# Kernel optimization log

Measured on AMD Instinct MI355X. Metric: run time of the kernel, lower is better.

## Reference

```python
import jax, jax.numpy as jnp
import numpy as np

N = 50000   # nodes
E = 800000  # edges (avg degree 16)
IN, H, OUT = 128, 128, 64


def setup_inputs() -> dict:
    key = jax.random.key(0)
    ks = jax.random.split(key, 8)

    def w(k, shape):
        fan_in = shape[0]
        return (jax.random.normal(k, shape, jnp.float32) / np.float32(np.sqrt(fan_in)))

    x = jax.random.normal(ks[0], (N, IN), jnp.float32)
    edge_index = jax.random.randint(ks[1], (2, E), 0, N, jnp.int64)
    return {
        "x": x,
        "edge_index": edge_index,
        "W1": w(ks[2], (IN, H)), "b1": jnp.zeros((H,), jnp.float32),
        "W2": w(ks[3], (H, H)),  "b2": jnp.zeros((H,), jnp.float32),
        "W3": w(ks[4], (H, H)),  "b3": jnp.zeros((H,), jnp.float32),
        "Wd1": w(ks[5], (H, H)), "bd1": jnp.zeros((H,), jnp.float32),
        "Wd2": w(ks[6], (H, OUT)), "bd2": jnp.zeros((OUT,), jnp.float32),
    }


def _gcn_conv(x, src, dst, norm, W, b):
    # x: [N, Cin] -> linear transform, gather along edges, normalized scatter-add
    h = x @ W                                   # [N, Cout]
    msg = h[src] * norm[:, None]                # [E+N, Cout]
    out = jax.ops.segment_sum(msg, dst, num_segments=N)
    return out + b


def reference(x, edge_index, W1, b1, W2, b2, W3, b3, Wd1, bd1, Wd2, bd2):
    # Add self-loops (PyG GCNConv default) and compute symmetric normalization.
    loops = jnp.arange(N, dtype=edge_index.dtype)
    src = jnp.concatenate([edge_index[0], loops])   # [E+N]
    dst = jnp.concatenate([edge_index[1], loops])   # [E+N]
    deg = jax.ops.segment_sum(jnp.ones_like(dst, dtype=x.dtype), dst, num_segments=N)
    dinv = jnp.where(deg > 0, jax.lax.rsqrt(deg), jnp.zeros_like(deg))
    norm = dinv[src] * dinv[dst]                    # [E+N]

    h = jax.nn.relu(_gcn_conv(x, src, dst, norm, W1, b1))
    h = jax.nn.relu(_gcn_conv(h, src, dst, norm, W2, b2))
    h = jax.nn.relu(_gcn_conv(h, src, dst, norm, W3, b3))

    h = jax.nn.relu(h @ Wd1 + bd1)
    return jax.nn.sigmoid(h @ Wd2 + bd2)            # [N, OUT]
```

## Files before the change

### kernel.cpp

```cpp
#include <hip/hip_runtime.h>
#include <hip/hip_bf16.h>
#include <hip/hip_fp16.h>

#define N_NODES 50000
#define N_EDGES 800000
#define C_H 128
#define C_OUT 64
#define NBLK 196
#define TSTRIDE 136
#define E_PAD 950272
#define MM_BLKS 782

typedef __attribute__((ext_vector_type(8))) short bf16x8;
typedef __attribute__((ext_vector_type(4))) float f32x4;

static __device__ __forceinline__ float bf_lo(unsigned int u) { return __uint_as_float(u << 16); }
static __device__ __forceinline__ float bf_hi(unsigned int u) { return __uint_as_float(u & 0xffff0000u); }
static __device__ __forceinline__ unsigned short f2bf(float f) {
    __hip_bfloat16 h = __float2bfloat16(f);
    return *(unsigned short*)&h;
}
static __device__ __forceinline__ unsigned int pack2(float a, float b) {
    return (unsigned int)f2bf(a) | ((unsigned int)f2bf(b) << 16);
}
static __device__ __forceinline__ unsigned short f2h_bits(float f) {
    union { __half h; unsigned short u; } c; c.h = __float2half_rn(f); return c.u;
}
static __device__ __forceinline__ float h_bits2f(unsigned short u) {
    union { __half h; unsigned short u; } c; c.u = u; return __half2float(c.h);
}

__global__ void prep_kernel(const int* __restrict__ dst, int* __restrict__ counts,
                            int* __restrict__ rank,
                            const float* __restrict__ W1, const float* __restrict__ W2,
                            const float* __restrict__ W3, const float* __restrict__ Wd1,
                            const float* __restrict__ Wd2,
                            unsigned short* __restrict__ P1, unsigned short* __restrict__ P2,
                            unsigned short* __restrict__ P3, unsigned short* __restrict__ Pd1,
                            unsigned short* __restrict__ Pd2,
                            unsigned int* __restrict__ epay) {
    int b = blockIdx.x;
    if (b < 3125) {
        int e = b * 256 + threadIdx.x;
        rank[e] = atomicAdd(&counts[dst[e]], 1);
    } else if (b < 3413) {
        int idx = (b - 3125) * 256 + threadIdx.x;
        if (idx < 4 * 16384) {
            int which = idx >> 14;
            int r = idx & 16383;
            const float* W = (which == 0) ? W1 : (which == 1) ? W2 : (which == 2) ? W3 : Wd1;
            unsigned short* P = (which == 0) ? P1 : (which == 1) ? P2 : (which == 2) ? P3 : Pd1;
            int j = r & 7, lane = (r >> 3) & 63, t = r >> 9;
            int nb = t & 7, kb = t >> 3;
            int k = kb * 32 + ((lane >> 4) << 3) + j;
            int n = nb * 16 + (lane & 15);
            P[r] = f2bf(W[(size_t)k * 128 + n]);
        } else {
            int r = idx - 65536;
            if (r < 8192) {
                int j = r & 7, lane = (r >> 3) & 63, t = r >> 9;
                int nb = t & 3, kb = t >> 2;
                int k = kb * 32 + ((lane >> 4) << 3) + j;
                int n = nb * 16 + (lane & 15);
                Pd2[r] = f2bf(Wd2[(size_t)k * 64 + n]);
            }
        }
    } else {
        int i = (b - 3413) * 256 + threadIdx.x;
        *(uint4*)(epay + (size_t)i * 4) = make_uint4(0, 0, 0, 0);
    }
}

__global__ void __launch_bounds__(256) scan1_kernel(const int* __restrict__ counts,
                                                    int* __restrict__ eblk,
                                                    int* __restrict__ bsum,
                                                    float* __restrict__ dinv) {
    __shared__ int ws[4];
    int i = blockIdx.x * 256 + threadIdx.x;
    int v = (i < N_NODES) ? counts[i] : 0;
    if (i < N_NODES) dinv[i] = rsqrtf((float)v + 1.0f);
    int vp = (v + 3) & ~3;
    int lane = threadIdx.x & 63, w = threadIdx.x >> 6;
    int x = vp;
    #pragma unroll
    for (int off = 1; off < 64; off <<= 1) {
        int t = __shfl_up(x, off, 64);
        if (lane >= off) x += t;
    }
    if (lane == 63) ws[w] = x;
    __syncthreads();
    if (threadIdx.x == 0) {
        int run = 0;
        #pragma unroll
        for (int k = 0; k < 4; ++k) { int t = ws[k]; ws[k] = run; run += t; }
        bsum[blockIdx.x] = run;
    }
    __syncthreads();
    if (i < N_NODES) eblk[i] = x - vp + ws[w];
}

__global__ void __launch_bounds__(256) scan2_kernel(const int* __restrict__ bsum,
                                                    int* __restrict__ bo,
                                                    int* __restrict__ rowptr) {
    __shared__ int ws[4];
    int i = threadIdx.x;
    int v = (i < NBLK) ? bsum[i] : 0;
    int lane = i & 63, w = i >> 6;
    int x = v;
    #pragma unroll
    for (int off = 1; off < 64; off <<= 1) {
        int t = __shfl_up(x, off, 64);
        if (lane >= off) x += t;
    }
    if (lane == 63) ws[w] = x;
    __syncthreads();
    if (i == 0) {
        int run = 0;
        #pragma unroll
        for (int k = 0; k < 4; ++k) { int t = ws[k]; ws[k] = run; run += t; }
    }
    __syncthreads();
    int excl = x - v + ws[w];
    if (i < NBLK) bo[i] = excl;
    if (i == 255) rowptr[N_NODES] = excl + v;
}

__global__ void scan3_kernel(const int* __restrict__ eblk, const int* __restrict__ bo,
                             int* __restrict__ rowptr) {
    int i = blockIdx.x * 256 + threadIdx.x;
    if (i < N_NODES) rowptr[i] = eblk[i] + bo[blockIdx.x];
}

__global__ void __launch_bounds__(256) fill_mm_kernel(
        const float* __restrict__ x, const unsigned short* __restrict__ P1,
        unsigned short* __restrict__ XW1,
        const int* __restrict__ src, const int* __restrict__ dst,
        const float* __restrict__ dinv,
        const int* __restrict__ rowptr, const int* __restrict__ rank,
        unsigned int* __restrict__ epay) {
    int b = blockIdx.x;
    if (b < MM_BLKS) {
        const int lane = threadIdx.x & 63;
        const int wave = threadIdx.x >> 6;
        const int wid  = b * 4 + wave;
        if (wid * 16 >= N_NODES) return;
        const int node = wid * 16 + (lane & 15);
        const int quad = lane >> 4;
        f32x4 acc[8];
        #pragma unroll
        for (int nb = 0; nb < 8; ++nb) acc[nb] = (f32x4){0.f, 0.f, 0.f, 0.f};
        #pragma unroll
        for (int kb = 0; kb < 4; ++kb) {
            const float* p = x + (size_t)node * 128 + kb * 32 + quad * 8;
            float4 lo = *(const float4*)p;
            float4 hi = *(const float4*)(p + 4);
            union { bf16x8 v; unsigned int u[4]; } tmp;
            tmp.u[0] = pack2(lo.x, lo.y); tmp.u[1] = pack2(lo.z, lo.w);
            tmp.u[2] = pack2(hi.x, hi.y); tmp.u[3] = pack2(hi.z, hi.w);
            #pragma unroll
            for (int nb = 0; nb < 8; ++nb) {
                bf16x8 wf = *(const bf16x8*)(P1 + ((size_t)(kb * 8 + nb) * 64 + lane) * 8);
                acc[nb] = __builtin_amdgcn_mfma_f32_16x16x32_bf16(wf, tmp.v, acc[nb], 0, 0, 0);
            }
        }
        #pragma unroll
        for (int nb = 0; nb < 8; ++nb) {
            int ch = nb * 16 + quad * 4;
            uint2 o;
            o.x = pack2(acc[nb][0], acc[nb][1]);
            o.y = pack2(acc[nb][2], acc[nb][3]);
            *(uint2*)(XW1 + (size_t)node * C_H + ch) = o;
        }
    } else {
        int e = (b - MM_BLKS) * 256 + threadIdx.x;
        if (e < N_EDGES) {
            int d = dst[e], s = src[e];
            int pos = rowptr[d] + rank[e];
            float nrm = dinv[s] * dinv[d];
            epay[pos] = (unsigned int)s | ((unsigned int)f2h_bits(nrm) << 16);
        }
    }
}

__global__ void __launch_bounds__(256) gather1_kernel(
        const int* __restrict__ rowptr,
        const unsigned int* __restrict__ epay,
        const float* __restrict__ dinv,
        const unsigned short* __restrict__ hin,
        const float* __restrict__ bias,
        unsigned short* __restrict__ out) {
    int t    = threadIdx.x;
    int node = blockIdx.x * 8 + (t >> 5);
    int c4   = (t & 31) << 2;

    float di = dinv[node], dii = di * di;
    uint2 raw = *(const uint2*)(hin + (size_t)node * C_H + c4);
    float a0 = bf_lo(raw.x) * dii, a1 = bf_hi(raw.x) * dii;
    float a2 = bf_lo(raw.y) * dii, a3 = bf_hi(raw.y) * dii;
    int beg = rowptr[node], end = rowptr[node + 1];
    int p = beg;
    for (; p + 8 <= end; p += 8) {
        uint4 ev0 = *(const uint4*)(epay + p);
        uint4 ev1 = *(const uint4*)(epay + p + 4);
        unsigned int ee[8] = {ev0.x, ev0.y, ev0.z, ev0.w, ev1.x, ev1.y, ev1.z, ev1.w};
        uint2 rv[8];
        #pragma unroll
        for (int j = 0; j < 8; ++j)
            rv[j] = *(const uint2*)(hin + (size_t)(ee[j] & 0xffffu) * C_H + c4);
        #pragma unroll
        for (int j = 0; j < 8; ++j) {
            float nm = h_bits2f((unsigned short)(ee[j] >> 16));
            a0 = fmaf(bf_lo(rv[j].x), nm, a0); a1 = fmaf(bf_hi(rv[j].x), nm, a1);
            a2 = fmaf(bf_lo(rv[j].y), nm, a2); a3 = fmaf(bf_hi(rv[j].y), nm, a3);
        }
    }
    if (p < end) {
        uint4 ev = *(const uint4*)(epay + p);
        unsigned int ee[4] = {ev.x, ev.y, ev.z, ev.w};
        uint2 rv[4];
        #pragma unroll
        for (int j = 0; j < 4; ++j)
            rv[j] = *(const uint2*)(hin + (size_t)(ee[j] & 0xffffu) * C_H + c4);
        #pragma unroll
        for (int j = 0; j < 4; ++j) {
            float nm = h_bits2f((unsigned short)(ee[j] >> 16));
            a0 = fmaf(bf_lo(rv[j].x), nm, a0); a1 = fmaf(bf_hi(rv[j].x), nm, a1);
            a2 = fmaf(bf_lo(rv[j].y), nm, a2); a3 = fmaf(bf_hi(rv[j].y), nm, a3);
        }
    }
    float4 ba = *(const float4*)(bias + c4);
    a0 = fmaxf(a0 + ba.x, 0.f); a1 = fmaxf(a1 + ba.y, 0.f);
    a2 = fmaxf(a2 + ba.z, 0.f); a3 = fmaxf(a3 + ba.w, 0.f);
    uint2 o;
    o.x = pack2(a0, a1); o.y = pack2(a2, a3);
    *(uint2*)(out + (size_t)node * C_H + c4) = o;
}

template <bool FINAL>
__global__ void __launch_bounds__(512) fused_layer_kernel(
        const int* __restrict__ rowptr,
        const unsigned int* __restrict__ epay,
        const float* __restrict__ dinv,
        const unsigned short* __restrict__ hin,
        const unsigned short* __restrict__ Wp,
        const float* __restrict__ bias,
        const unsigned short* __restrict__ Wd1p,
        const float* __restrict__ bd1,
        const unsigned short* __restrict__ Wd2p,
        const float* __restrict__ bd2,
        unsigned short* __restrict__ out_b,
        float* __restrict__ out_f) {
    __shared__ unsigned short sG[16 * TSTRIDE];
    const int t = threadIdx.x;

    {
        int nl = t >> 5, c4 = (t & 31) << 2;
        int node = blockIdx.x * 16 + nl;
        float di = dinv[node], dii = di * di;
        uint2 raw = *(const uint2*)(hin + (size_t)node * C_H + c4);
        float a0 = bf_lo(raw.x) * dii, a1 = bf_hi(raw.x) * dii;
        float a2 = bf_lo(raw.y) * dii, a3 = bf_hi(raw.y) * dii;
        int beg = rowptr[node], end = rowptr[node + 1];
        int p = beg;
        for (; p + 8 <= end; p += 8) {
            uint4 ev0 = *(const uint4*)(epay + p);
            uint4 ev1 = *(const uint4*)(epay + p + 4);
            unsigned int ee[8] = {ev0.x, ev0.y, ev0.z, ev0.w, ev1.x, ev1.y, ev1.z, ev1.w};
            uint2 rv[8];
            #pragma unroll
            for (int j = 0; j < 8; ++j)
                rv[j] = *(const uint2*)(hin + (size_t)(ee[j] & 0xffffu) * C_H + c4);
            #pragma unroll
            for (int j = 0; j < 8; ++j) {
                float nm = h_bits2f((unsigned short)(ee[j] >> 16));
                a0 = fmaf(bf_lo(rv[j].x), nm, a0); a1 = fmaf(bf_hi(rv[j].x), nm, a1);
                a2 = fmaf(bf_lo(rv[j].y), nm, a2); a3 = fmaf(bf_hi(rv[j].y), nm, a3);
            }
        }
        if (p < end) {
            uint4 ev = *(const uint4*)(epay + p);
            unsigned int ee[4] = {ev.x, ev.y, ev.z, ev.w};
            uint2 rv[4];
            #pragma unroll
            for (int j = 0; j < 4; ++j)
                rv[j] = *(const uint2*)(hin + (size_t)(ee[j] & 0xffffu) * C_H + c4);
            #pragma unroll
            for (int j = 0; j < 4; ++j) {
                float nm = h_bits2f((unsigned short)(ee[j] >> 16));
                a0 = fmaf(bf_lo(rv[j].x), nm, a0); a1 = fmaf(bf_hi(rv[j].x), nm, a1);
                a2 = fmaf(bf_lo(rv[j].y), nm, a2); a3 = fmaf(bf_hi(rv[j].y), nm, a3);
            }
        }
        uint2 o;
        o.x = pack2(a0, a1); o.y = pack2(a2, a3);
        *(uint2*)(sG + nl * TSTRIDE + c4) = o;
    }
    __syncthreads();

    const int lane = t & 63, wave = t >> 6, quad = lane >> 4, row = lane & 15;
    const int node = blockIdx.x * 16 + row;
    const int nb = wave;

    f32x4 acc0 = (f32x4){0.f, 0.f, 0.f, 0.f};
    #pragma unroll
    for (int kb = 0; kb < 4; ++kb) {
        bf16x8 hf = *(const bf16x8*)(sG + row * TSTRIDE + kb * 32 + quad * 8);
        bf16x8 wf0 = *(const bf16x8*)(Wp + ((size_t)(kb * 8 + nb) * 64 + lane) * 8);
        acc0 = __builtin_amdgcn_mfma_f32_16x16x32_bf16(wf0, hf, acc0, 0, 0, 0);
    }
    float4 ba0 = *(const float4*)(bias + nb * 16 + quad * 4);
    float v00 = fmaxf(acc0[0] + ba0.x, 0.f), v01 = fmaxf(acc0[1] + ba0.y, 0.f);
    float v02 = fmaxf(acc0[2] + ba0.z, 0.f), v03 = fmaxf(acc0[3] + ba0.w, 0.f);

    if (!FINAL) {
        uint2 o0;
        o0.x = pack2(v00, v01); o0.y = pack2(v02, v03);
        *(uint2*)(out_b + (size_t)node * C_H + nb * 16 + quad * 4) = o0;
        return;
    }

    __syncthreads();
    {
        uint2 o0;
        o0.x = pack2(v00, v01); o0.y = pack2(v02, v03);
        *(uint2*)(sG + row * TSTRIDE + nb * 16 + quad * 4) = o0;
    }
    __syncthreads();

    acc0 = (f32x4){0.f, 0.f, 0.f, 0.f};
    #pragma unroll
    for (int kb = 0; kb < 4; ++kb) {
        bf16x8 hf = *(const bf16x8*)(sG + row * TSTRIDE + kb * 32 + quad * 8);
        bf16x8 wf0 = *(const bf16x8*)(Wd1p + ((size_t)(kb * 8 + nb) * 64 + lane) * 8);
        acc0 = __builtin_amdgcn_mfma_f32_16x16x32_bf16(wf0, hf, acc0, 0, 0, 0);
    }
    ba0 = *(const float4*)(bd1 + nb * 16 + quad * 4);
    v00 = fmaxf(acc0[0] + ba0.x, 0.f); v01 = fmaxf(acc0[1] + ba0.y, 0.f);
    v02 = fmaxf(acc0[2] + ba0.z, 0.f); v03 = fmaxf(acc0[3] + ba0.w, 0.f);
    __syncthreads();
    {
        uint2 o0;
        o0.x = pack2(v00, v01); o0.y = pack2(v02, v03);
        *(uint2*)(sG + row * TSTRIDE + nb * 16 + quad * 4) = o0;
    }
    __syncthreads();

    if (wave < 4) {
        f32x4 acc = (f32x4){0.f, 0.f, 0.f, 0.f};
        #pragma unroll
        for (int kb = 0; kb < 4; ++kb) {
            bf16x8 hf = *(const bf16x8*)(sG + row * TSTRIDE + kb * 32 + quad * 8);
            bf16x8 wf = *(const bf16x8*)(Wd2p + ((size_t)(kb * 4 + wave) * 64 + lane) * 8);
            acc = __builtin_amdgcn_mfma_f32_16x16x32_bf16(wf, hf, acc, 0, 0, 0);
        }
        int ch = wave * 16 + quad * 4;
        float4 b4 = *(const float4*)(bd2 + ch);
        float4 r;
        r.x = 1.f / (1.f + expf(-(acc[0] + b4.x)));
        r.y = 1.f / (1.f + expf(-(acc[1] + b4.y)));
        r.z = 1.f / (1.f + expf(-(acc[2] + b4.z)));
        r.w = 1.f / (1.f + expf(-(acc[3] + b4.w)));
        *(float4*)(out_f + (size_t)node * C_OUT + ch) = r;
    }
}

extern "C" void kernel_launch(void* const* d_in, const int* in_sizes, int n_in,
                              void* d_out, int out_size, void* d_ws, size_t ws_size,
                              hipStream_t stream) {
    const float* x   = (const float*)d_in[0];
    const int*   ei  = (const int*)d_in[1];
    const float* W1  = (const float*)d_in[2];
    const float* b1  = (const float*)d_in[3];
    const float* W2  = (const float*)d_in[4];
    const float* b2  = (const float*)d_in[5];
    const float* W3  = (const float*)d_in[6];
    const float* b3  = (const float*)d_in[7];
    const float* Wd1 = (const float*)d_in[8];
    const float* bd1 = (const float*)d_in[9];
    const float* Wd2 = (const float*)d_in[10];
    const float* bd2 = (const float*)d_in[11];

    const int* src = ei;
    const int* dst = ei + N_EDGES;

    char* base = (char*)d_ws;
    size_t off = 0;
    auto alloc = [&](size_t bytes) { char* p = base + off; off += (bytes + 255) & ~size_t(255); return p; };
    int*            counts = (int*)alloc(50176 * 4);
    unsigned int*   epay   = (unsigned int*)alloc((size_t)E_PAD * 4);
    int*            rank   = (int*)alloc((size_t)N_EDGES * 4);
    float*          dinv   = (float*)alloc(N_NODES * 4);
    int*            rowptr = (int*)alloc((N_NODES + 1) * 4);
    int*            eblk   = (int*)alloc(N_NODES * 4);
    int*            bsum   = (int*)alloc(256 * 4);
    int*            bo     = (int*)alloc(256 * 4);
    unsigned short* XW1    = (unsigned short*)alloc((size_t)N_NODES * C_H * 2);
    unsigned short* bufA   = (unsigned short*)alloc((size_t)N_NODES * C_H * 2);
    unsigned short* bufB   = (unsigned short*)alloc((size_t)N_NODES * C_H * 2);
    unsigned short* P1     = (unsigned short*)alloc(128 * 128 * 2);
    unsigned short* P2     = (unsigned short*)alloc(128 * 128 * 2);
    unsigned short* P3     = (unsigned short*)alloc(128 * 128 * 2);
    unsigned short* Pd1    = (unsigned short*)alloc(128 * 128 * 2);
    unsigned short* Pd2    = (unsigned short*)alloc(128 * 64 * 2);

    const int T = 256;
    dim3 blk(T);
    dim3 blk512(512);
    dim3 gN((N_NODES + T - 1) / T);
    dim3 gPrep(3125 + 288 + 928);
    dim3 gFillMM(MM_BLKS + 3125);
    dim3 gG1(N_NODES / 8);
    dim3 gFused(N_NODES / 16);

    hipMemsetAsync(counts, 0, 50176 * 4, stream);
    prep_kernel<<<gPrep, blk, 0, stream>>>(dst, counts, rank,
                                           W1, W2, W3, Wd1, Wd2,
                                           P1, P2, P3, Pd1, Pd2, epay);
    scan1_kernel<<<gN, blk, 0, stream>>>(counts, eblk, bsum, dinv);
    scan2_kernel<<<1, blk, 0, stream>>>(bsum, bo, rowptr);
    scan3_kernel<<<gN, blk, 0, stream>>>(eblk, bo, rowptr);
    fill_mm_kernel<<<gFillMM, blk, 0, stream>>>(x, P1, XW1, src, dst, dinv,
                                                rowptr, rank, epay);

    gather1_kernel<<<gG1, blk, 0, stream>>>(rowptr, epay, dinv, XW1, b1, bufA);
    fused_layer_kernel<false><<<gFused, blk512, 0, stream>>>(
        rowptr, epay, dinv, bufA, P2, b2, nullptr, nullptr, nullptr, nullptr, bufB, nullptr);
    fused_layer_kernel<true><<<gFused, blk512, 0, stream>>>(
        rowptr, epay, dinv, bufB, P3, b3, Pd1, bd1, Pd2, bd2, nullptr, (float*)d_out);
}
```

Baseline: 256.9 us.

## Split fused aggregate-matmul layers and slice aggregation by channel quarters

Replaces the fused aggregate-then-transform kernels with separate transform-then-aggregate passes: a standalone MFMA matmul kernel, a gather kernel and a head kernel. The gather kernel now splits the 128 channels into four 32-channel slices across the grid, with 8 threads per node. The aim is to shrink the working set per gather pass so neighbor rows are reused better in cache, and to free the gather from the matmul's register and LDS pressure. In exchange it adds kernel launches and extra full-size intermediate round trips through global memory, and each edge payload is now read four times.

```diff
diff --git a/kernel.cpp b/kernel.cpp
--- a/kernel.cpp
+++ b/kernel.cpp
@@ -10,6 +10,7 @@
 #define TSTRIDE 136
 #define E_PAD 950272
 #define MM_BLKS 782
+#define AGG_BLKS 1563
 
 typedef __attribute__((ext_vector_type(8))) short bf16x8;
 typedef __attribute__((ext_vector_type(4))) float f32x4;
@@ -182,16 +183,20 @@
     }
 }
 
-__global__ void __launch_bounds__(256) gather1_kernel(
+__global__ void __launch_bounds__(256) agg_kernel(
         const int* __restrict__ rowptr,
         const unsigned int* __restrict__ epay,
         const float* __restrict__ dinv,
         const unsigned short* __restrict__ hin,
         const float* __restrict__ bias,
         unsigned short* __restrict__ out) {
-    int t    = threadIdx.x;
-    int node = blockIdx.x * 8 + (t >> 5);
-    int c4   = (t & 31) << 2;
+    const unsigned int bx = blockIdx.x;
+    const unsigned int slice = bx / AGG_BLKS;
+    const unsigned int nblk  = bx - slice * AGG_BLKS;
+    const int t = threadIdx.x;
+    const int node = nblk * 32 + (t >> 3);
+    if (node >= N_NODES) return;
+    const int c4 = slice * 32 + (t & 7) * 4;
 
     float di = dinv[node], dii = di * di;
     uint2 raw = *(const uint2*)(hin + (size_t)node * C_H + c4);
@@ -236,64 +241,49 @@
     *(uint2*)(out + (size_t)node * C_H + c4) = o;
 }
 
-template <bool FINAL>
-__global__ void __launch_bounds__(512) fused_layer_kernel(
-        const int* __restrict__ rowptr,
-        const unsigned int* __restrict__ epay,
-        const float* __restrict__ dinv,
+__global__ void __launch_bounds__(256) mm_kernel(
         const unsigned short* __restrict__ hin,
         const unsigned short* __restrict__ Wp,
-        const float* __restrict__ bias,
-        const unsigned short* __restrict__ Wd1p,
-        const float* __restrict__ bd1,
-        const unsigned short* __restrict__ Wd2p,
-        const float* __restrict__ bd2,
-        unsigned short* __restrict__ out_b,
+        unsigned short* __restrict__ out) {
+    const int lane = threadIdx.x & 63;
+    const int wave = threadIdx.x >> 6;
+    const int wid  = blockIdx.x * 4 + wave;
+    if (wid * 16 >= N_NODES) return;
+    const int node = wid * 16 + (lane & 15);
+    const int quad = lane >> 4;
+    f32x4 acc[8];
+    #pragma unroll
+    for (int nb = 0; nb < 8; ++nb) acc[nb] = (f32x4){0.f, 0.f, 0.f, 0.f};
+    #pragma unroll
+    for (int kb = 0; kb < 4; ++kb) {
+        bf16x8 hf = *(const bf16x8*)(hin + (size_t)node * C_H + kb * 32 + quad * 8);
+        #pragma unroll
+        for (int nb = 0; nb < 8; ++nb) {
+            bf16x8 wf = *(const bf16x8*)(Wp + ((size_t)(kb * 8 + nb) * 64 + lane) * 8);
+            acc[nb] = __builtin_amdgcn_mfma_f32_16x16x32_bf16(wf, hf, acc[nb], 0, 0, 0);
+        }
+    }
+    #pragma unroll
+    for (int nb = 0; nb < 8; ++nb) {
+        int ch = nb * 16 + quad * 4;
+        uint2 o;
+        o.x = pack2(acc[nb][0], acc[nb][1]);
+        o.y = pack2(acc[nb][2], acc[nb][3]);
+        *(uint2*)(out + (size_t)node * C_H + ch) = o;
+    }
+}
+
+__global__ void __launch_bounds__(512) head_kernel(
+        const unsigned short* __restrict__ hin,
+        const unsigned short* __restrict__ Wd1p, const float* __restrict__ bd1,
+        const unsigned short* __restrict__ Wd2p, const float* __restrict__ bd2,
         float* __restrict__ out_f) {
     __shared__ unsigned short sG[16 * TSTRIDE];
     const int t = threadIdx.x;
-
     {
         int nl = t >> 5, c4 = (t & 31) << 2;
         int node = blockIdx.x * 16 + nl;
-        float di = dinv[node], dii = di * di;
-        uint2 raw = *(const uint2*)(hin + (size_t)node * C_H + c4);
-        float a0 = bf_lo(raw.x) * dii, a1 = bf_hi(raw.x) * dii;
-        float a2 = bf_lo(raw.y) * dii, a3 = bf_hi(raw.y) * dii;
-        int beg = rowptr[node], end = rowptr[node + 1];
-        int p = beg;
-        for (; p + 8 <= end; p += 8) {
-            uint4 ev0 = *(const uint4*)(epay + p);
-            uint4 ev1 = *(const uint4*)(epay + p + 4);
-            unsigned int ee[8] = {ev0.x, ev0.y, ev0.z, ev0.w, ev1.x, ev1.y, ev1.z, ev1.w};
-            uint2 rv[8];
-            #pragma unroll
-            for (int j = 0; j < 8; ++j)
-                rv[j] = *(const uint2*)(hin + (size_t)(ee[j] & 0xffffu) * C_H + c4);
-            #pragma unroll
-            for (int j = 0; j < 8; ++j) {
-                float nm = h_bits2f((unsigned short)(ee[j] >> 16));
-                a0 = fmaf(bf_lo(rv[j].x), nm, a0); a1 = fmaf(bf_hi(rv[j].x), nm, a1);
-                a2 = fmaf(bf_lo(rv[j].y), nm, a2); a3 = fmaf(bf_hi(rv[j].y), nm, a3);
-            }
-        }
-        if (p < end) {
-            uint4 ev = *(const uint4*)(epay + p);
-            unsigned int ee[4] = {ev.x, ev.y, ev.z, ev.w};
-            uint2 rv[4];
-            #pragma unroll
-            for (int j = 0; j < 4; ++j)
-                rv[j] = *(const uint2*)(hin + (size_t)(ee[j] & 0xffffu) * C_H + c4);
-            #pragma unroll
-            for (int j = 0; j < 4; ++j) {
-                float nm = h_bits2f((unsigned short)(ee[j] >> 16));
-                a0 = fmaf(bf_lo(rv[j].x), nm, a0); a1 = fmaf(bf_hi(rv[j].x), nm, a1);
-                a2 = fmaf(bf_lo(rv[j].y), nm, a2); a3 = fmaf(bf_hi(rv[j].y), nm, a3);
-            }
-        }
-        uint2 o;
-        o.x = pack2(a0, a1); o.y = pack2(a2, a3);
-        *(uint2*)(sG + nl * TSTRIDE + c4) = o;
+        *(uint2*)(sG + nl * TSTRIDE + c4) = *(const uint2*)(hin + (size_t)node * C_H + c4);
     }
     __syncthreads();
 
@@ -302,41 +292,15 @@
     const int nb = wave;
 
     f32x4 acc0 = (f32x4){0.f, 0.f, 0.f, 0.f};
-    #pragma unroll
-    for (int kb = 0; kb < 4; ++kb) {
-        bf16x8 hf = *(const bf16x8*)(sG + row * TSTRIDE + kb * 32 + quad * 8);
-        bf16x8 wf0 = *(const bf16x8*)(Wp + ((size_t)(kb * 8 + nb) * 64 + lane) * 8);
-        acc0 = __builtin_amdgcn_mfma_f32_16x16x32_bf16(wf0, hf, acc0, 0, 0, 0);
-    }
-    float4 ba0 = *(const float4*)(bias + nb * 16 + quad * 4);
-    float v00 = fmaxf(acc0[0] + ba0.x, 0.f), v01 = fmaxf(acc0[1] + ba0.y, 0.f);
-    float v02 = fmaxf(acc0[2] + ba0.z, 0.f), v03 = fmaxf(acc0[3] + ba0.w, 0.f);
-
-    if (!FINAL) {
-        uint2 o0;
-        o0.x = pack2(v00, v01); o0.y = pack2(v02, v03);
-        *(uint2*)(out_b + (size_t)node * C_H + nb * 16 + quad * 4) = o0;
-        return;
-    }
-
-    __syncthreads();
-    {
-        uint2 o0;
-        o0.x = pack2(v00, v01); o0.y = pack2(v02, v03);
-        *(uint2*)(sG + row * TSTRIDE + nb * 16 + quad * 4) = o0;
-    }
-    __syncthreads();
-
-    acc0 = (f32x4){0.f, 0.f, 0.f, 0.f};
     #pragma unroll
     for (int kb = 0; kb < 4; ++kb) {
         bf16x8 hf = *(const bf16x8*)(sG + row * TSTRIDE + kb * 32 + quad * 8);
         bf16x8 wf0 = *(const bf16x8*)(Wd1p + ((size_t)(kb * 8 + nb) * 64 + lane) * 8);
         acc0 = __builtin_amdgcn_mfma_f32_16x16x32_bf16(wf0, hf, acc0, 0, 0, 0);
     }
-    ba0 = *(const float4*)(bd1 + nb * 16 + quad * 4);
-    v00 = fmaxf(acc0[0] + ba0.x, 0.f); v01 = fmaxf(acc0[1] + ba0.y, 0.f);
-    v02 = fmaxf(acc0[2] + ba0.z, 0.f); v03 = fmaxf(acc0[3] + ba0.w, 0.f);
+    float4 ba0 = *(const float4*)(bd1 + nb * 16 + quad * 4);
+    float v00 = fmaxf(acc0[0] + ba0.x, 0.f), v01 = fmaxf(acc0[1] + ba0.y, 0.f);
+    float v02 = fmaxf(acc0[2] + ba0.z, 0.f), v03 = fmaxf(acc0[3] + ba0.w, 0.f);
     __syncthreads();
     {
         uint2 o0;
@@ -409,8 +373,9 @@
     dim3 gN((N_NODES + T - 1) / T);
     dim3 gPrep(3125 + 288 + 928);
     dim3 gFillMM(MM_BLKS + 3125);
-    dim3 gG1(N_NODES / 8);
-    dim3 gFused(N_NODES / 16);
+    dim3 gAgg(4 * AGG_BLKS);
+    dim3 gMM(MM_BLKS);
+    dim3 gHead(N_NODES / 16);
 
     hipMemsetAsync(counts, 0, 50176 * 4, stream);
     prep_kernel<<<gPrep, blk, 0, stream>>>(dst, counts, rank,
@@ -422,9 +387,10 @@
     fill_mm_kernel<<<gFillMM, blk, 0, stream>>>(x, P1, XW1, src, dst, dinv,
                                                 rowptr, rank, epay);
 
-    gather1_kernel<<<gG1, blk, 0, stream>>>(rowptr, epay, dinv, XW1, b1, bufA);
-    fused_layer_kernel<false><<<gFused, blk512, 0, stream>>>(
-        rowptr, epay, dinv, bufA, P2, b2, nullptr, nullptr, nullptr, nullptr, bufB, nullptr);
-    fused_layer_kernel<true><<<gFused, blk512, 0, stream>>>(
-        rowptr, epay, dinv, bufB, P3, b3, Pd1, bd1, Pd2, bd2, nullptr, (float*)d_out);
-}
+    agg_kernel<<<gAgg, blk, 0, stream>>>(rowptr, epay, dinv, XW1, b1, bufA);
+    mm_kernel<<<gMM, blk, 0, stream>>>(bufA, P2, XW1);
+    agg_kernel<<<gAgg, blk, 0, stream>>>(rowptr, epay, dinv, XW1, b2, bufB);
+    mm_kernel<<<gMM, blk, 0, stream>>>(bufB, P3, bufA);
+    agg_kernel<<<gAgg, blk, 0, stream>>>(rowptr, epay, dinv, bufA, b3, XW1);
+    head_kernel<<<gHead, blk512, 0, stream>>>(XW1, Pd1, bd1, Pd2, bd2, (float*)d_out);
+}
```

Result: slower. 314.1 us (+22.3%).
